# Performance work log

Hardware: AMD Instinct MI355X
Metric: run time of the kernel (lower is better)

## Reference

```python
import jax, jax.numpy as jnp
import numpy as np

N = 100000
E = 1600000
DIN = 256
DOUT = 64


def setup_inputs() -> dict:
    key = jax.random.key(0)
    ks = jax.random.split(key, 12)
    s = 1.0 / np.sqrt(DIN)
    so = 1.0 / np.sqrt(DOUT)
    return {
        "x": jax.random.normal(ks[0], (N, DIN), dtype=jnp.float32),
        "edge_index": jax.random.randint(ks[1], (2, E), 0, N, dtype=jnp.int32),
        "W_hp": jax.random.uniform(ks[2], (DIN, DOUT), jnp.float32, -s, s),
        "b_hp": jnp.zeros((DOUT,), jnp.float32),
        "W_lp": jax.random.uniform(ks[3], (DIN, DOUT), jnp.float32, -s, s),
        "b_lp": jnp.zeros((DOUT,), jnp.float32),
        "W_i": jax.random.uniform(ks[4], (DIN, DOUT), jnp.float32, -s, s),
        "b_i": jnp.zeros((DOUT,), jnp.float32),
        "w_h": jax.random.uniform(ks[5], (DOUT, 1), jnp.float32, -so, so),
        "b_h": jnp.zeros((1,), jnp.float32),
        "w_l": jax.random.uniform(ks[6], (DOUT, 1), jnp.float32, -so, so),
        "b_l": jnp.zeros((1,), jnp.float32),
        "w_i2": jax.random.uniform(ks[7], (DOUT, 1), jnp.float32, -so, so),
        "b_i2": jnp.zeros((1,), jnp.float32),
    }


def _gcn_norm(edge_index, n):
    # add self loops, symmetric GCN normalization
    ar = jnp.arange(n, dtype=edge_index.dtype)
    src = jnp.concatenate([edge_index[0], ar])
    dst = jnp.concatenate([edge_index[1], ar])
    deg = jax.ops.segment_sum(jnp.ones_like(dst, dtype=jnp.float32), dst, num_segments=n)
    dinv = jnp.where(deg > 0, jax.lax.rsqrt(jnp.maximum(deg, 1e-12)), 0.0)
    norm = dinv[src] * dinv[dst]  # [E+N]
    return src, dst, norm


def reference(x, edge_index, W_hp, b_hp, W_lp, b_lp, W_i, b_i,
              w_h, b_h, w_l, b_l, w_i2, b_i2):
    n = x.shape[0]
    src, dst, norm = _gcn_norm(edge_index, n)

    def prop(h):  # Ahat @ h via gather-scale-scatter
        return jax.ops.segment_sum(h[src] * norm[:, None], dst, num_segments=n)

    # three ACM-GCN filter branches
    xw_hp = x @ W_hp + b_hp
    H_hp = jax.nn.relu(xw_hp - prop(xw_hp))      # high-pass: (I - Ahat) X W
    H_lp = jax.nn.relu(prop(x @ W_lp + b_lp))    # low-pass:  Ahat X W
    H_i = jax.nn.relu(x @ W_i + b_i)             # identity:  X W

    # per-node sigmoid gates (mix=False path)
    a_h = jax.nn.sigmoid(H_hp @ w_h + b_h)[:, 0]
    a_l = jax.nn.sigmoid(H_lp @ w_l + b_l)[:, 0]
    a_i = jax.nn.sigmoid(H_i @ w_i2 + b_i2)[:, 0]

    # diag(alpha) @ H == broadcasted row scaling (same math, no NxN diag)
    out = a_h[:, None] * H_hp + a_l[:, None] * H_lp + a_i[:, None] * H_i
    return jax.nn.log_softmax(out, axis=1)
```

## Files before the change

kernel.cpp:

```cpp
#include <hip/hip_runtime.h>
#include <hip/hip_bf16.h>
#include <hip/hip_fp16.h>
#include <math.h>

#define DIN 256
#define DOUT 64

#define BKT_CAP 1408
#define C1_CAP 36864
#define CH1 2048
#define CH2 4096
#define NB2_PER 9

typedef __attribute__((ext_vector_type(8))) short bfrag8;
typedef __attribute__((ext_vector_type(4))) float ffrag4;
typedef __fp16 fp16x2 __attribute__((ext_vector_type(2)));

#define AS1 __attribute__((address_space(1)))
#define AS3 __attribute__((address_space(3)))

__device__ inline unsigned short f2bf(float f) {
    union { float f; unsigned u; } v; v.f = f;
    unsigned r = v.u + 0x7FFF + ((v.u >> 16) & 1);
    return (unsigned short)(r >> 16);
}
__device__ inline unsigned cvt2(float a, float b) {
    unsigned r;
    asm("v_cvt_pk_bf16_f32 %0, %1, %2" : "=v"(r) : "v"(a), "v"(b));
    return r;
}

__device__ inline float wave_sum(float v) {
    #pragma unroll
    for (int off = 32; off > 0; off >>= 1) v += __shfl_xor(v, off, 64);
    return v;
}
__device__ inline float wave_max(float v) {
    #pragma unroll
    for (int off = 32; off > 0; off >>= 1) v = fmaxf(v, __shfl_xor(v, off, 64));
    return v;
}

__device__ inline void gload16(const void* g, void* l) {
    __builtin_amdgcn_global_load_lds((const AS1 void*)g, (AS3 void*)l, 16, 0, 0);
}

union HU { unsigned u; __half2 h; };

__device__ inline void prew_body(int id, const float* __restrict__ Whp,
                                 const float* __restrict__ Wlp,
                                 const float* __restrict__ Wi,
                                 unsigned* __restrict__ wt) {
    if (id >= 8 * 192 * 4) return;
    int p = id & 3;
    int col = (id >> 2) % 192;
    int kci = id / (192 * 4);
    int s = p ^ ((col >> 1) & 3);
    int m = col >> 6, c = col & 63;
    const float* W = (m == 0) ? Whp : ((m == 1) ? Wlp : Wi);
    int k0 = kci * 32 + s * 4;
    unsigned o0 = (unsigned)f2bf(W[(k0 + 0) * 64 + c]) | ((unsigned)f2bf(W[(k0 + 1) * 64 + c]) << 16);
    unsigned o1 = (unsigned)f2bf(W[(k0 + 2) * 64 + c]) | ((unsigned)f2bf(W[(k0 + 3) * 64 + c]) << 16);
    unsigned o2 = (unsigned)f2bf(W[(k0 + 16) * 64 + c]) | ((unsigned)f2bf(W[(k0 + 17) * 64 + c]) << 16);
    unsigned o3 = (unsigned)f2bf(W[(k0 + 18) * 64 + c]) | ((unsigned)f2bf(W[(k0 + 19) * 64 + c]) << 16);
    uint4 v; v.x = o0; v.y = o1; v.z = o2; v.w = o3;
    *(uint4*)&wt[(size_t)id * 4] = v;
}

__global__ __launch_bounds__(256) void k_bin1(
    const int* __restrict__ src, const int* __restrict__ dst, int E,
    int* __restrict__ gcnt1, unsigned* __restrict__ cwords,
    const float* __restrict__ Whp, const float* __restrict__ Wlp,
    const float* __restrict__ Wi, unsigned* __restrict__ wt) {
    __shared__ int hist[4][64];
    __shared__ int roff[4][64];
    __shared__ int loff[64], gb[64];
    __shared__ unsigned words[CH1];
    __shared__ unsigned char aux[CH1];
    int t = threadIdx.x;
    int rep = t & 3;
    int base = blockIdx.x * CH1;
    int nloc = E - base;
    if (nloc > CH1) nloc = CH1;
    if (nloc < 0) nloc = 0;
    if (t < 64) { hist[0][t] = 0; hist[1][t] = 0; hist[2][t] = 0; hist[3][t] = 0; }
    __syncthreads();
    unsigned myw[8];
    short myr[8];
    signed char myb[8];
    #pragma unroll
    for (int i = 0; i < 8; ++i) {
        int idx = i * 256 + t;
        myb[i] = -1;
        if (idx < nloc) {
            int s = src[base + idx], d = dst[base + idx];
            int b = d >> 11;
            myw[i] = (unsigned)s | ((unsigned)(d & 2047) << 17);
            myb[i] = (signed char)b;
            myr[i] = (short)atomicAdd(&hist[rep][b], 1);
        }
    }
    __syncthreads();
    if (t < 64) {
        int run = 0;
        #pragma unroll
        for (int r = 0; r < 4; ++r) { roff[r][t] = run; run += hist[r][t]; }
        int v = run;
        int x = v;
        #pragma unroll
        for (int off = 1; off < 64; off <<= 1) {
            int y = __shfl_up(x, off, 64);
            if (t >= off) x += y;
        }
        loff[t] = x - v;
        gb[t] = v ? atomicAdd(&gcnt1[t], v) : 0;
    }
    __syncthreads();
    #pragma unroll
    for (int i = 0; i < 8; ++i) {
        if (myb[i] >= 0) {
            int b = myb[i];
            int pos = loff[b] + roff[rep][b] + myr[i];
            words[pos] = myw[i];
            aux[pos] = (unsigned char)b;
        }
    }
    __syncthreads();
    for (int j = t; j < nloc; j += 256) {
        int b = aux[j];
        int g = gb[b] + (j - loff[b]);
        if (g < C1_CAP) cwords[(size_t)b * C1_CAP + g] = words[j];
    }
    if (blockIdx.x < 24) prew_body(blockIdx.x * 256 + t, Whp, Wlp, Wi, wt);
}

__global__ __launch_bounds__(256) void k_bin2(
    const int* __restrict__ gcnt1, const unsigned* __restrict__ cwords,
    int* __restrict__ gcnt2, unsigned* __restrict__ bwords,
    int* __restrict__ cnt, int N) {
    __shared__ int hist[32], loff[32], gb[32];
    __shared__ int hist2k[2048];
    __shared__ unsigned words[CH2];
    __shared__ unsigned char aux[CH2];
    int t = threadIdx.x;
    int b = blockIdx.x / NB2_PER, j = blockIdx.x % NB2_PER;
    int tot = gcnt1[b];
    if (tot > C1_CAP) tot = C1_CAP;
    int base = j * CH2;
    int nloc = tot - base;
    if (nloc <= 0) return;
    if (nloc > CH2) nloc = CH2;
    if (t < 32) hist[t] = 0;
    for (int i = t; i < 2048; i += 256) hist2k[i] = 0;
    __syncthreads();
    unsigned myw[16];
    short myr[16];
    signed char myf[16];
    const unsigned* cw = cwords + (size_t)b * C1_CAP + base;
    #pragma unroll
    for (int i = 0; i < 16; ++i) {
        int idx = i * 256 + t;
        myf[i] = -1;
        if (idx < nloc) {
            unsigned w = cw[idx];
            int ld = (int)(w >> 17);
            int f = ld >> 6;
            myw[i] = (w & 0x1FFFF) | ((unsigned)(ld & 63) << 17);
            myf[i] = (signed char)f;
            myr[i] = (short)atomicAdd(&hist[f], 1);
            atomicAdd(&hist2k[ld], 1);
        }
    }
    __syncthreads();
    if (t < 32) {
        int v = hist[t];
        int x = v;
        #pragma unroll
        for (int off = 1; off < 32; off <<= 1) {
            int y = __shfl_up(x, off, 64);
            if (t >= off) x += y;
        }
        loff[t] = x - v;
        gb[t] = v ? atomicAdd(&gcnt2[b * 32 + t], v) : 0;
    }
    __syncthreads();
    #pragma unroll
    for (int i = 0; i < 16; ++i) {
        if (myf[i] >= 0) {
            int pos = loff[myf[i]] + myr[i];
            words[pos] = myw[i];
            aux[pos] = (unsigned char)myf[i];
        }
    }
    __syncthreads();
    for (int j2 = t; j2 < nloc; j2 += 256) {
        int f = aux[j2];
        int g = gb[f] + (j2 - loff[f]);
        if (g < BKT_CAP) bwords[(size_t)(b * 32 + f) * BKT_CAP + g] = words[j2];
    }
    int nbase = b * 2048;
    for (int i = t; i < 2048; i += 256) {
        int c = hist2k[i];
        if (c && nbase + i < N) atomicAdd(&cnt[nbase + i], c);
    }
}

__global__ __launch_bounds__(256) void k_gemm(
    const float* __restrict__ x, int N,
    const unsigned* __restrict__ wt,
    const float* __restrict__ bhp, const float* __restrict__ blp,
    const float* __restrict__ bi, const int* __restrict__ cnt,
    unsigned* __restrict__ xws, __half* __restrict__ xwi) {
    __shared__ __attribute__((aligned(16))) float Al[128 * 32];
    __shared__ __attribute__((aligned(16))) unsigned short Bl[192 * 32];
    int t = threadIdx.x;
    int wave = t >> 6, lane = t & 63;
    int l15 = lane & 15, lhi = lane >> 4;
    int row0 = blockIdx.x * 128;

    ffrag4 acc[2][12];
    #pragma unroll
    for (int mf = 0; mf < 2; ++mf)
        #pragma unroll
        for (int nf = 0; nf < 12; ++nf)
            acc[mf][nf] = (ffrag4){0.f, 0.f, 0.f, 0.f};

    int arow[4], achk[4];
    #pragma unroll
    for (int i = 0; i < 4; ++i) {
        int off = i * 4096 + t * 16;
        int r = off >> 7;
        int cp = (off >> 4) & 7;
        arow[i] = row0 + r < N ? row0 + r : N - 1;
        achk[i] = cp ^ (r & 7);
    }

    for (int kci = 0; kci < 8; ++kci) {
        #pragma unroll
        for (int i = 0; i < 4; ++i)
            gload16(x + (size_t)arow[i] * DIN + kci * 32 + achk[i] * 4,
                    (char*)Al + i * 4096 + wave * 1024);
        #pragma unroll
        for (int i = 0; i < 3; ++i)
            gload16(wt + (size_t)kci * 3072 + ((i * 4096 + t * 16) >> 2),
                    (char*)Bl + i * 4096 + wave * 1024);
        __syncthreads();

        union { bfrag8 v; unsigned u[4]; } af[2];
        #pragma unroll
        for (int mf = 0; mf < 2; ++mf) {
            int row = wave * 32 + mf * 16 + l15;
            int p1 = lhi ^ (row & 7);
            float4 lo = ((const float4*)Al)[row * 8 + p1];
            float4 hi = ((const float4*)Al)[row * 8 + (p1 ^ 4)];
            af[mf].u[0] = cvt2(lo.x, lo.y);
            af[mf].u[1] = cvt2(lo.z, lo.w);
            af[mf].u[2] = cvt2(hi.x, hi.y);
            af[mf].u[3] = cvt2(hi.z, hi.w);
        }
        bfrag8 bfr[12];
        #pragma unroll
        for (int nf = 0; nf < 12; ++nf) {
            int col = nf * 16 + l15;
            int p = lhi ^ ((col >> 1) & 3);
            bfr[nf] = *((const bfrag8*)Bl + col * 4 + p);
        }
        #pragma unroll
        for (int mf = 0; mf < 2; ++mf)
            #pragma unroll
            for (int nf = 0; nf < 12; ++nf)
                acc[mf][nf] = __builtin_amdgcn_mfma_f32_16x16x32_bf16(
                    af[mf].v, bfr[nf], acc[mf][nf], 0, 0, 0);
        __syncthreads();
    }

    #pragma unroll
    for (int mf = 0; mf < 2; ++mf) {
        #pragma unroll
        for (int nf = 0; nf < 4; ++nf) {
            int col = nf * 16 + l15;
            float bh_ = bhp[col], bl_ = blp[col], bi_ = bi[col];
            #pragma unroll
            for (int r = 0; r < 4; ++r) {
                int grow = row0 + wave * 32 + mf * 16 + lhi * 4 + r;
                if (grow >= N) continue;
                float dv = rsqrtf((float)cnt[grow] + 1.f);
                float hp = (acc[mf][nf][r] + bh_) * dv;
                float lp = (acc[mf][nf + 4][r] + bl_) * dv;
                union { fp16x2 p; unsigned u; } pu;
                pu.p = __builtin_amdgcn_cvt_pkrtz(hp, lp);
                xws[(size_t)grow * 64 + col] = pu.u;
                xwi[(size_t)grow * 64 + col] = __float2half(acc[mf][nf + 8][r] + bi_);
            }
        }
    }
}

__global__ __launch_bounds__(256) void k_bagg(
    const int* __restrict__ gcnt2, const unsigned* __restrict__ bwords,
    const unsigned* __restrict__ xws, const __half* __restrict__ xwi,
    const float* __restrict__ wh, const float* __restrict__ bh,
    const float* __restrict__ wl, const float* __restrict__ bl,
    const float* __restrict__ wi2, const float* __restrict__ bi2,
    float* __restrict__ out, int N) {
    __shared__ unsigned sorted[1024];
    __shared__ int h2[32], lo2[32];
    int t = threadIdx.x, bb = blockIdx.x;
    int b = bb >> 1, half = bb & 1;
    int n0 = b * 64 + half * 32;
    if (n0 >= N) return;
    int cntE = gcnt2[b];
    if (cntE > BKT_CAP) cntE = BKT_CAP;
    if (t < 32) h2[t] = 0;
    __syncthreads();
    unsigned mw[6];
    short ml[6], mr[6];
    #pragma unroll
    for (int i = 0; i < 6; ++i) {
        int idx = i * 256 + t;
        ml[i] = -1;
        if (idx < cntE) {
            unsigned w = bwords[(size_t)b * BKT_CAP + idx];
            int ld = (int)(w >> 17);
            if ((ld >> 5) == half) {
                int l5 = ld & 31;
                mw[i] = (w & 0x1FFFF) << 8;
                ml[i] = (short)l5;
                mr[i] = (short)atomicAdd(&h2[l5], 1);
            }
        }
    }
    __syncthreads();
    if (t < 32) {
        int v = h2[t];
        int x = v;
        #pragma unroll
        for (int off = 1; off < 32; off <<= 1) {
            int y = __shfl_up(x, off, 64);
            if (t >= off) x += y;
        }
        lo2[t] = x - v;
    }
    __syncthreads();
    #pragma unroll
    for (int i = 0; i < 6; ++i)
        if (ml[i] >= 0) {
            int pos = lo2[ml[i]] + mr[i];
            if (pos < 1024) sorted[pos] = mw[i];
        }
    __syncthreads();

    int wave = t >> 6, lane = t & 63;
    int h = lane >> 5, f2 = lane & 31;
    const unsigned laneoff = (unsigned)(f2 * 8);
    const char* bp = (const char*)xws;
    float wh0 = wh[f2 * 2], wh1 = wh[f2 * 2 + 1];
    float wl0 = wl[f2 * 2], wl1 = wl[f2 * 2 + 1];
    float wi0 = wi2[f2 * 2], wi1 = wi2[f2 * 2 + 1];
    float bhv = bh[0], blv = bl[0], biv = bi2[0];
    for (int ni = 0; ni < 8; ++ni) {
        int ln = wave * 8 + ni;
        int node = n0 + ln;
        if (node >= N) break;
        int c = h2[ln], e0 = lo2[ln], e1 = e0 + c;
        if (e1 > 1024) e1 = 1024;
        unsigned long long us = *(const unsigned long long*)(bp + ((unsigned)node << 8) + laneoff);
        HU z; z.u = 0;
        __half2 a0a = z.h, a0b = z.h, a1a = z.h, a1b = z.h;
        int e = e0;
        for (; e + 16 <= e1; e += 16) {
            unsigned long long v[8];
            #pragma unroll
            for (int k = 0; k < 8; ++k)
                v[k] = *(const unsigned long long*)(bp + (sorted[e + 2 * k + h] + laneoff));
            #pragma unroll
            for (int k = 0; k < 8; k += 2) {
                HU a, bq, c2, d2;
                a.u = (unsigned)v[k];      bq.u = (unsigned)(v[k] >> 32);
                c2.u = (unsigned)v[k + 1]; d2.u = (unsigned)(v[k + 1] >> 32);
                a0a = __hadd2(a0a, a.h);  a1a = __hadd2(a1a, bq.h);
                a0b = __hadd2(a0b, c2.h); a1b = __hadd2(a1b, d2.h);
            }
        }
        if (e + 8 <= e1) {
            unsigned long long v[4];
            #pragma unroll
            for (int k = 0; k < 4; ++k)
                v[k] = *(const unsigned long long*)(bp + (sorted[e + 2 * k + h] + laneoff));
            #pragma unroll
            for (int k = 0; k < 4; k += 2) {
                HU a, bq, c2, d2;
                a.u = (unsigned)v[k];      bq.u = (unsigned)(v[k] >> 32);
                c2.u = (unsigned)v[k + 1]; d2.u = (unsigned)(v[k + 1] >> 32);
                a0a = __hadd2(a0a, a.h);  a1a = __hadd2(a1a, bq.h);
                a0b = __hadd2(a0b, c2.h); a1b = __hadd2(a1b, d2.h);
            }
            e += 8;
        }
        if (e + 4 <= e1) {
            unsigned long long v[2];
            #pragma unroll
            for (int k = 0; k < 2; ++k)
                v[k] = *(const unsigned long long*)(bp + (sorted[e + 2 * k + h] + laneoff));
            HU a, bq, c2, d2;
            a.u = (unsigned)v[0];  bq.u = (unsigned)(v[0] >> 32);
            c2.u = (unsigned)v[1]; d2.u = (unsigned)(v[1] >> 32);
            a0a = __hadd2(a0a, a.h);  a1a = __hadd2(a1a, bq.h);
            a0b = __hadd2(a0b, c2.h); a1b = __hadd2(a1b, d2.h);
            e += 4;
        }
        for (; e < e1; e += 2) {
            int ei = e + h;
            if (ei < e1) {
                unsigned long long v = *(const unsigned long long*)(bp + (sorted[ei] + laneoff));
                HU a, bq;
                a.u = (unsigned)v;
                bq.u = (unsigned)(v >> 32);
                a0a = __hadd2(a0a, a.h);
                a1a = __hadd2(a1a, bq.h);
            }
        }
        __half2 acc0 = __hadd2(a0a, a0b);
        __half2 acc1 = __hadd2(a1a, a1b);
        HU c0, c1;
        c0.h = acc0; c0.u = __shfl_xor(c0.u, 32, 64);
        c1.h = acc1; c1.u = __shfl_xor(c1.u, 32, 64);
        acc0 = __hadd2(acc0, c0.h);
        acc1 = __hadd2(acc1, c1.h);
        float s_h0 = __low2float(acc0), s_l0 = __high2float(acc0);
        float s_h1 = __low2float(acc1), s_l1 = __high2float(acc1);
        float fc = (float)c + 1.f;
        float dv = rsqrtf(fc), sq = sqrtf(fc);
        HU q0, q1;
        q0.u = (unsigned)us; q1.u = (unsigned)(us >> 32);
        float xh0 = __low2float(q0.h), xl0 = __high2float(q0.h);
        float xh1 = __low2float(q1.h), xl1 = __high2float(q1.h);
        float Hh0 = fmaxf(xh0 * sq - dv * (s_h0 + xh0), 0.f);
        float Hh1 = fmaxf(xh1 * sq - dv * (s_h1 + xh1), 0.f);
        float Hl0 = fmaxf(dv * (s_l0 + xl0), 0.f);
        float Hl1 = fmaxf(dv * (s_l1 + xl1), 0.f);
        HU qi;
        qi.u = *(const unsigned*)((const char*)xwi + ((size_t)node * 128) + f2 * 4);
        float Hi0 = fmaxf(__low2float(qi.h), 0.f);
        float Hi1 = fmaxf(__high2float(qi.h), 0.f);
        float zh = 0.5f * wave_sum(Hh0 * wh0 + Hh1 * wh1) + bhv;
        float zl = 0.5f * wave_sum(Hl0 * wl0 + Hl1 * wl1) + blv;
        float zi = 0.5f * wave_sum(Hi0 * wi0 + Hi1 * wi1) + biv;
        float ah = 1.f / (1.f + expf(-zh));
        float al = 1.f / (1.f + expf(-zl));
        float ai = 1.f / (1.f + expf(-zi));
        float o0 = ah * Hh0 + al * Hl0 + ai * Hi0;
        float o1 = ah * Hh1 + al * Hl1 + ai * Hi1;
        float mx = wave_max(fmaxf(o0, o1));
        float ss = 0.5f * wave_sum(expf(o0 - mx) + expf(o1 - mx));
        float lse = mx + logf(ss);
        if (h == 0) {
            float2 r; r.x = o0 - lse; r.y = o1 - lse;
            *(float2*)&out[(size_t)node * 64 + f2 * 2] = r;
        }
    }
}

extern "C" void kernel_launch(void* const* d_in, const int* in_sizes, int n_in,
                              void* d_out, int out_size, void* d_ws, size_t ws_size,
                              hipStream_t stream) {
    const float* x   = (const float*)d_in[0];
    const int*   ei  = (const int*)d_in[1];
    const float* Whp = (const float*)d_in[2];
    const float* bhp = (const float*)d_in[3];
    const float* Wlp = (const float*)d_in[4];
    const float* blp = (const float*)d_in[5];
    const float* Wi  = (const float*)d_in[6];
    const float* bi  = (const float*)d_in[7];
    const float* wh  = (const float*)d_in[8];
    const float* bh  = (const float*)d_in[9];
    const float* wl  = (const float*)d_in[10];
    const float* bl  = (const float*)d_in[11];
    const float* wi2 = (const float*)d_in[12];
    const float* bi2 = (const float*)d_in[13];
    float* out = (float*)d_out;

    int N = in_sizes[0] / DIN;
    int E = in_sizes[1] / 2;
    const int* src = ei;
    const int* dst = ei + E;
    int nc = (N + 2047) >> 11;
    int nbuck2 = nc * 32;

    char* w = (char*)d_ws;
    size_t off = 0;
    auto alloc = [&](size_t bytes) {
        void* p = w + off;
        off += (bytes + 255) & ~size_t(255);
        return p;
    };
    int*      cnt    = (int*)alloc((size_t)N * 4);
    int*      gcnt1  = (int*)alloc(64 * 4);
    int*      gcnt2  = (int*)alloc((size_t)nbuck2 * 4);
    size_t    zero_end = off;
    unsigned* cwords = (unsigned*)alloc((size_t)nc * C1_CAP * 4);
    unsigned* bwords = (unsigned*)alloc((size_t)nbuck2 * BKT_CAP * 4);
    unsigned* xws    = (unsigned*)alloc((size_t)N * 64 * 4);
    __half*   xwi    = (__half*)alloc((size_t)N * 64 * 2);
    unsigned* wt     = (unsigned*)alloc((size_t)8 * 192 * 4 * 16);
    (void)ws_size; (void)n_in; (void)out_size;

    hipError_t e0 = hipMemsetAsync(cnt, 0, zero_end, stream); (void)e0;
    k_bin1<<<(E + CH1 - 1) / CH1, 256, 0, stream>>>(src, dst, E, gcnt1, cwords,
                                                    Whp, Wlp, Wi, wt);
    k_bin2<<<nc * NB2_PER, 256, 0, stream>>>(gcnt1, cwords, gcnt2, bwords, cnt, N);
    k_gemm<<<(N + 127) / 128, 256, 0, stream>>>(x, N, wt, bhp, blp, bi, cnt,
                                                xws, xwi);
    k_bagg<<<nbuck2 * 2, 256, 0, stream>>>(gcnt2, bwords, xws, xwi,
                                           wh, bh, wl, bl, wi2, bi2, out, N);
}
```

Measured before the change: 150.7 us.

## Replace two-pass edge binning with single-pass 1024-bucket sort and per-edge source norm

Collapses the two-level radix binning (64 coarse then 32 fine buckets) into one pass that bins edges directly into 128-node buckets, counting in-degree with global atomics per edge. The GEMM no longer scales by the destination norm; instead a new kernel builds packed fp16 source dinv values, and aggregation multiplies each gathered row by its source dinv via hfma2, with the destination scale applied at the end. Aggregation blocks grow to 512 threads handling 128 nodes. The weight preprocessing moves to its own launch. This removes a full read/write of the intermediate edge buffer, at the cost of 1.6M global atomics on cnt, two extra kernel launches, a larger LDS scan and an extra LDS array per edge in aggregation.

```diff
diff --git a/kernel.cpp b/kernel.cpp
--- a/kernel.cpp
+++ b/kernel.cpp
@@ -6,11 +6,9 @@
 #define DIN 256
 #define DOUT 64
 
-#define BKT_CAP 1408
-#define C1_CAP 36864
-#define CH1 2048
-#define CH2 4096
-#define NB2_PER 9
+#define CH1 4096
+#define NBK 1024
+#define MCAP 2560
 
 typedef __attribute__((ext_vector_type(8))) short bfrag8;
 typedef __attribute__((ext_vector_type(4))) float ffrag4;
@@ -47,10 +45,9 @@
 
 union HU { unsigned u; __half2 h; };
 
-__device__ inline void prew_body(int id, const float* __restrict__ Whp,
-                                 const float* __restrict__ Wlp,
-                                 const float* __restrict__ Wi,
-                                 unsigned* __restrict__ wt) {
+__global__ void k_prew(const float* __restrict__ Whp, const float* __restrict__ Wlp,
+                       const float* __restrict__ Wi, unsigned* __restrict__ wt) {
+    int id = blockIdx.x * 256 + threadIdx.x;
     if (id >= 8 * 192 * 4) return;
     int p = id & 3;
     int col = (id >> 2) % 192;
@@ -67,141 +64,77 @@
     *(uint4*)&wt[(size_t)id * 4] = v;
 }
 
-__global__ __launch_bounds__(256) void k_bin1(
+__global__ __launch_bounds__(512) void k_bin1(
     const int* __restrict__ src, const int* __restrict__ dst, int E,
-    int* __restrict__ gcnt1, unsigned* __restrict__ cwords,
-    const float* __restrict__ Whp, const float* __restrict__ Wlp,
-    const float* __restrict__ Wi, unsigned* __restrict__ wt) {
-    __shared__ int hist[4][64];
-    __shared__ int roff[4][64];
-    __shared__ int loff[64], gb[64];
+    int* __restrict__ cnt, int* __restrict__ gcnt, unsigned* __restrict__ mwords) {
+    __shared__ int hist[NBK], loff[NBK], gb[NBK];
+    __shared__ int sc[512];
     __shared__ unsigned words[CH1];
-    __shared__ unsigned char aux[CH1];
+    __shared__ unsigned short aux[CH1];
     int t = threadIdx.x;
-    int rep = t & 3;
     int base = blockIdx.x * CH1;
     int nloc = E - base;
     if (nloc > CH1) nloc = CH1;
     if (nloc < 0) nloc = 0;
-    if (t < 64) { hist[0][t] = 0; hist[1][t] = 0; hist[2][t] = 0; hist[3][t] = 0; }
+    for (int i = t; i < NBK; i += 512) hist[i] = 0;
     __syncthreads();
     unsigned myw[8];
-    short myr[8];
-    signed char myb[8];
+    short myr[8], myb[8];
     #pragma unroll
     for (int i = 0; i < 8; ++i) {
-        int idx = i * 256 + t;
+        int idx = i * 512 + t;
         myb[i] = -1;
         if (idx < nloc) {
             int s = src[base + idx], d = dst[base + idx];
-            int b = d >> 11;
-            myw[i] = (unsigned)s | ((unsigned)(d & 2047) << 17);
-            myb[i] = (signed char)b;
-            myr[i] = (short)atomicAdd(&hist[rep][b], 1);
-        }
-    }
-    __syncthreads();
-    if (t < 64) {
-        int run = 0;
-        #pragma unroll
-        for (int r = 0; r < 4; ++r) { roff[r][t] = run; run += hist[r][t]; }
-        int v = run;
-        int x = v;
-        #pragma unroll
-        for (int off = 1; off < 64; off <<= 1) {
-            int y = __shfl_up(x, off, 64);
-            if (t >= off) x += y;
-        }
-        loff[t] = x - v;
-        gb[t] = v ? atomicAdd(&gcnt1[t], v) : 0;
+            int b = d >> 7;
+            myw[i] = (unsigned)s | ((unsigned)(d & 127) << 17);
+            myb[i] = (short)b;
+            myr[i] = (short)atomicAdd(&hist[b], 1);
+            atomicAdd(&cnt[d], 1);
+        }
+    }
+    __syncthreads();
+    int part = hist[t * 2] + hist[t * 2 + 1];
+    sc[t] = part; __syncthreads();
+    for (int off = 1; off < 512; off <<= 1) {
+        int x = (t >= off) ? sc[t - off] : 0;
+        __syncthreads();
+        sc[t] += x;
+        __syncthreads();
+    }
+    int run = sc[t] - part;
+    loff[t * 2] = run;
+    run += hist[t * 2];
+    loff[t * 2 + 1] = run;
+    __syncthreads();
+    for (int i = t; i < NBK; i += 512) {
+        int c = hist[i];
+        gb[i] = c ? atomicAdd(&gcnt[i], c) : 0;
     }
     __syncthreads();
     #pragma unroll
     for (int i = 0; i < 8; ++i) {
         if (myb[i] >= 0) {
-            int b = myb[i];
-            int pos = loff[b] + roff[rep][b] + myr[i];
+            int pos = loff[myb[i]] + myr[i];
             words[pos] = myw[i];
-            aux[pos] = (unsigned char)b;
-        }
-    }
-    __syncthreads();
-    for (int j = t; j < nloc; j += 256) {
+            aux[pos] = (unsigned short)myb[i];
+        }
+    }
+    __syncthreads();
+    for (int j = t; j < nloc; j += 512) {
         int b = aux[j];
         int g = gb[b] + (j - loff[b]);
-        if (g < C1_CAP) cwords[(size_t)b * C1_CAP + g] = words[j];
-    }
-    if (blockIdx.x < 24) prew_body(blockIdx.x * 256 + t, Whp, Wlp, Wi, wt);
-}
-
-__global__ __launch_bounds__(256) void k_bin2(
-    const int* __restrict__ gcnt1, const unsigned* __restrict__ cwords,
-    int* __restrict__ gcnt2, unsigned* __restrict__ bwords,
-    int* __restrict__ cnt, int N) {
-    __shared__ int hist[32], loff[32], gb[32];
-    __shared__ int hist2k[2048];
-    __shared__ unsigned words[CH2];
-    __shared__ unsigned char aux[CH2];
-    int t = threadIdx.x;
-    int b = blockIdx.x / NB2_PER, j = blockIdx.x % NB2_PER;
-    int tot = gcnt1[b];
-    if (tot > C1_CAP) tot = C1_CAP;
-    int base = j * CH2;
-    int nloc = tot - base;
-    if (nloc <= 0) return;
-    if (nloc > CH2) nloc = CH2;
-    if (t < 32) hist[t] = 0;
-    for (int i = t; i < 2048; i += 256) hist2k[i] = 0;
-    __syncthreads();
-    unsigned myw[16];
-    short myr[16];
-    signed char myf[16];
-    const unsigned* cw = cwords + (size_t)b * C1_CAP + base;
-    #pragma unroll
-    for (int i = 0; i < 16; ++i) {
-        int idx = i * 256 + t;
-        myf[i] = -1;
-        if (idx < nloc) {
-            unsigned w = cw[idx];
-            int ld = (int)(w >> 17);
-            int f = ld >> 6;
-            myw[i] = (w & 0x1FFFF) | ((unsigned)(ld & 63) << 17);
-            myf[i] = (signed char)f;
-            myr[i] = (short)atomicAdd(&hist[f], 1);
-            atomicAdd(&hist2k[ld], 1);
-        }
-    }
-    __syncthreads();
-    if (t < 32) {
-        int v = hist[t];
-        int x = v;
-        #pragma unroll
-        for (int off = 1; off < 32; off <<= 1) {
-            int y = __shfl_up(x, off, 64);
-            if (t >= off) x += y;
-        }
-        loff[t] = x - v;
-        gb[t] = v ? atomicAdd(&gcnt2[b * 32 + t], v) : 0;
-    }
-    __syncthreads();
-    #pragma unroll
-    for (int i = 0; i < 16; ++i) {
-        if (myf[i] >= 0) {
-            int pos = loff[myf[i]] + myr[i];
-            words[pos] = myw[i];
-            aux[pos] = (unsigned char)myf[i];
-        }
-    }
-    __syncthreads();
-    for (int j2 = t; j2 < nloc; j2 += 256) {
-        int f = aux[j2];
-        int g = gb[f] + (j2 - loff[f]);
-        if (g < BKT_CAP) bwords[(size_t)(b * 32 + f) * BKT_CAP + g] = words[j2];
-    }
-    int nbase = b * 2048;
-    for (int i = t; i < 2048; i += 256) {
-        int c = hist2k[i];
-        if (c && nbase + i < N) atomicAdd(&cnt[nbase + i], c);
+        if (g < MCAP) mwords[(size_t)b * MCAP + g] = words[j];
+    }
+}
+
+__global__ void k_dinv2(const int* __restrict__ cnt, unsigned* __restrict__ dinv2, int N) {
+    int i = blockIdx.x * blockDim.x + threadIdx.x;
+    if (i < N) {
+        float dv = rsqrtf((float)cnt[i] + 1.f);
+        union { fp16x2 p; unsigned u; } pu;
+        pu.p = __builtin_amdgcn_cvt_pkrtz(dv, dv);
+        dinv2[i] = pu.u;
     }
 }
 
@@ -209,7 +142,7 @@
     const float* __restrict__ x, int N,
     const unsigned* __restrict__ wt,
     const float* __restrict__ bhp, const float* __restrict__ blp,
-    const float* __restrict__ bi, const int* __restrict__ cnt,
+    const float* __restrict__ bi,
     unsigned* __restrict__ xws, __half* __restrict__ xwi) {
     __shared__ __attribute__((aligned(16))) float Al[128 * 32];
     __shared__ __attribute__((aligned(16))) unsigned short Bl[192 * 32];
@@ -284,9 +217,8 @@
             for (int r = 0; r < 4; ++r) {
                 int grow = row0 + wave * 32 + mf * 16 + lhi * 4 + r;
                 if (grow >= N) continue;
-                float dv = rsqrtf((float)cnt[grow] + 1.f);
-                float hp = (acc[mf][nf][r] + bh_) * dv;
-                float lp = (acc[mf][nf + 4][r] + bl_) * dv;
+                float hp = acc[mf][nf][r] + bh_;
+                float lp = acc[mf][nf + 4][r] + bl_;
                 union { fp16x2 p; unsigned u; } pu;
                 pu.p = __builtin_amdgcn_cvt_pkrtz(hp, lp);
                 xws[(size_t)grow * 64 + col] = pu.u;
@@ -296,57 +228,57 @@
     }
 }
 
-__global__ __launch_bounds__(256) void k_bagg(
-    const int* __restrict__ gcnt2, const unsigned* __restrict__ bwords,
+__global__ __launch_bounds__(512) void k_bagg(
+    const int* __restrict__ gcnt, const unsigned* __restrict__ mwords,
     const unsigned* __restrict__ xws, const __half* __restrict__ xwi,
+    const unsigned* __restrict__ dinv2,
     const float* __restrict__ wh, const float* __restrict__ bh,
     const float* __restrict__ wl, const float* __restrict__ bl,
     const float* __restrict__ wi2, const float* __restrict__ bi2,
     float* __restrict__ out, int N) {
-    __shared__ unsigned sorted[1024];
-    __shared__ int h2[32], lo2[32];
-    int t = threadIdx.x, bb = blockIdx.x;
-    int b = bb >> 1, half = bb & 1;
-    int n0 = b * 64 + half * 32;
+    __shared__ unsigned sorted[MCAP];
+    __shared__ unsigned sdv[MCAP];
+    __shared__ int h2[128], lo2[128], sc2[128];
+    int t = threadIdx.x, b = blockIdx.x;
+    int n0 = b << 7;
     if (n0 >= N) return;
-    int cntE = gcnt2[b];
-    if (cntE > BKT_CAP) cntE = BKT_CAP;
-    if (t < 32) h2[t] = 0;
-    __syncthreads();
-    unsigned mw[6];
-    short ml[6], mr[6];
-    #pragma unroll
-    for (int i = 0; i < 6; ++i) {
-        int idx = i * 256 + t;
+    int cntE = gcnt[b];
+    if (cntE > MCAP) cntE = MCAP;
+    if (t < 128) h2[t] = 0;
+    __syncthreads();
+    unsigned mw[5];
+    short ml[5], mr[5];
+    #pragma unroll
+    for (int i = 0; i < 5; ++i) {
+        int idx = i * 512 + t;
         ml[i] = -1;
         if (idx < cntE) {
-            unsigned w = bwords[(size_t)b * BKT_CAP + idx];
+            unsigned w = mwords[(size_t)b * MCAP + idx];
             int ld = (int)(w >> 17);
-            if ((ld >> 5) == half) {
-                int l5 = ld & 31;
-                mw[i] = (w & 0x1FFFF) << 8;
-                ml[i] = (short)l5;
-                mr[i] = (short)atomicAdd(&h2[l5], 1);
-            }
-        }
-    }
-    __syncthreads();
-    if (t < 32) {
-        int v = h2[t];
-        int x = v;
-        #pragma unroll
-        for (int off = 1; off < 32; off <<= 1) {
-            int y = __shfl_up(x, off, 64);
-            if (t >= off) x += y;
-        }
-        lo2[t] = x - v;
-    }
-    __syncthreads();
-    #pragma unroll
-    for (int i = 0; i < 6; ++i)
+            mw[i] = (w & 0x1FFFF) << 8;
+            ml[i] = (short)ld;
+            mr[i] = (short)atomicAdd(&h2[ld], 1);
+        }
+    }
+    __syncthreads();
+    if (t < 128) sc2[t] = h2[t];
+    __syncthreads();
+    for (int off = 1; off < 128; off <<= 1) {
+        int x = (t < 128 && t >= off) ? sc2[t - off] : 0;
+        __syncthreads();
+        if (t < 128) sc2[t] += x;
+        __syncthreads();
+    }
+    if (t < 128) lo2[t] = sc2[t] - h2[t];
+    __syncthreads();
+    #pragma unroll
+    for (int i = 0; i < 5; ++i)
         if (ml[i] >= 0) {
             int pos = lo2[ml[i]] + mr[i];
-            if (pos < 1024) sorted[pos] = mw[i];
+            if (pos < MCAP) {
+                sorted[pos] = mw[i];
+                sdv[pos] = dinv2[mw[i] >> 8];
+            }
         }
     __syncthreads();
 
@@ -358,66 +290,82 @@
     float wl0 = wl[f2 * 2], wl1 = wl[f2 * 2 + 1];
     float wi0 = wi2[f2 * 2], wi1 = wi2[f2 * 2 + 1];
     float bhv = bh[0], blv = bl[0], biv = bi2[0];
-    for (int ni = 0; ni < 8; ++ni) {
-        int ln = wave * 8 + ni;
+    for (int ni = 0; ni < 16; ++ni) {
+        int ln = wave * 16 + ni;
         int node = n0 + ln;
         if (node >= N) break;
         int c = h2[ln], e0 = lo2[ln], e1 = e0 + c;
-        if (e1 > 1024) e1 = 1024;
+        if (e1 > MCAP) e1 = MCAP;
         unsigned long long us = *(const unsigned long long*)(bp + ((unsigned)node << 8) + laneoff);
         HU z; z.u = 0;
         __half2 a0a = z.h, a0b = z.h, a1a = z.h, a1b = z.h;
         int e = e0;
         for (; e + 16 <= e1; e += 16) {
             unsigned long long v[8];
-            #pragma unroll
-            for (int k = 0; k < 8; ++k)
-                v[k] = *(const unsigned long long*)(bp + (sorted[e + 2 * k + h] + laneoff));
+            unsigned dd[8];
+            #pragma unroll
+            for (int k = 0; k < 8; ++k) {
+                int idx = e + 2 * k + h;
+                dd[k] = sdv[idx];
+                v[k] = *(const unsigned long long*)(bp + (sorted[idx] + laneoff));
+            }
             #pragma unroll
             for (int k = 0; k < 8; k += 2) {
-                HU a, bq, c2, d2;
+                HU a, bq, c2, d2, w0, w1;
                 a.u = (unsigned)v[k];      bq.u = (unsigned)(v[k] >> 32);
                 c2.u = (unsigned)v[k + 1]; d2.u = (unsigned)(v[k + 1] >> 32);
-                a0a = __hadd2(a0a, a.h);  a1a = __hadd2(a1a, bq.h);
-                a0b = __hadd2(a0b, c2.h); a1b = __hadd2(a1b, d2.h);
+                w0.u = dd[k]; w1.u = dd[k + 1];
+                a0a = __hfma2(a.h, w0.h, a0a);  a1a = __hfma2(bq.h, w0.h, a1a);
+                a0b = __hfma2(c2.h, w1.h, a0b); a1b = __hfma2(d2.h, w1.h, a1b);
             }
         }
         if (e + 8 <= e1) {
             unsigned long long v[4];
-            #pragma unroll
-            for (int k = 0; k < 4; ++k)
-                v[k] = *(const unsigned long long*)(bp + (sorted[e + 2 * k + h] + laneoff));
+            unsigned dd[4];
+            #pragma unroll
+            for (int k = 0; k < 4; ++k) {
+                int idx = e + 2 * k + h;
+                dd[k] = sdv[idx];
+                v[k] = *(const unsigned long long*)(bp + (sorted[idx] + laneoff));
+            }
             #pragma unroll
             for (int k = 0; k < 4; k += 2) {
-                HU a, bq, c2, d2;
+                HU a, bq, c2, d2, w0, w1;
                 a.u = (unsigned)v[k];      bq.u = (unsigned)(v[k] >> 32);
                 c2.u = (unsigned)v[k + 1]; d2.u = (unsigned)(v[k + 1] >> 32);
-                a0a = __hadd2(a0a, a.h);  a1a = __hadd2(a1a, bq.h);
-                a0b = __hadd2(a0b, c2.h); a1b = __hadd2(a1b, d2.h);
+                w0.u = dd[k]; w1.u = dd[k + 1];
+                a0a = __hfma2(a.h, w0.h, a0a);  a1a = __hfma2(bq.h, w0.h, a1a);
+                a0b = __hfma2(c2.h, w1.h, a0b); a1b = __hfma2(d2.h, w1.h, a1b);
             }
             e += 8;
         }
         if (e + 4 <= e1) {
             unsigned long long v[2];
-            #pragma unroll
-            for (int k = 0; k < 2; ++k)
-                v[k] = *(const unsigned long long*)(bp + (sorted[e + 2 * k + h] + laneoff));
-            HU a, bq, c2, d2;
+            unsigned dd[2];
+            #pragma unroll
+            for (int k = 0; k < 2; ++k) {
+                int idx = e + 2 * k + h;
+                dd[k] = sdv[idx];
+                v[k] = *(const unsigned long long*)(bp + (sorted[idx] + laneoff));
+            }
+            HU a, bq, c2, d2, w0, w1;
             a.u = (unsigned)v[0];  bq.u = (unsigned)(v[0] >> 32);
             c2.u = (unsigned)v[1]; d2.u = (unsigned)(v[1] >> 32);
-            a0a = __hadd2(a0a, a.h);  a1a = __hadd2(a1a, bq.h);
-            a0b = __hadd2(a0b, c2.h); a1b = __hadd2(a1b, d2.h);
+            w0.u = dd[0]; w1.u = dd[1];
+            a0a = __hfma2(a.h, w0.h, a0a);  a1a = __hfma2(bq.h, w0.h, a1a);
+            a0b = __hfma2(c2.h, w1.h, a0b); a1b = __hfma2(d2.h, w1.h, a1b);
             e += 4;
         }
         for (; e < e1; e += 2) {
             int ei = e + h;
             if (ei < e1) {
                 unsigned long long v = *(const unsigned long long*)(bp + (sorted[ei] + laneoff));
-                HU a, bq;
+                HU a, bq, w0;
                 a.u = (unsigned)v;
                 bq.u = (unsigned)(v >> 32);
-                a0a = __hadd2(a0a, a.h);
-                a1a = __hadd2(a1a, bq.h);
+                w0.u = sdv[ei];
+                a0a = __hfma2(a.h, w0.h, a0a);
+                a1a = __hfma2(bq.h, w0.h, a1a);
             }
         }
         __half2 acc0 = __hadd2(a0a, a0b);
@@ -429,16 +377,15 @@
         acc1 = __hadd2(acc1, c1.h);
         float s_h0 = __low2float(acc0), s_l0 = __high2float(acc0);
         float s_h1 = __low2float(acc1), s_l1 = __high2float(acc1);
-        float fc = (float)c + 1.f;
-        float dv = rsqrtf(fc), sq = sqrtf(fc);
+        float dv = rsqrtf((float)c + 1.f);
         HU q0, q1;
         q0.u = (unsigned)us; q1.u = (unsigned)(us >> 32);
         float xh0 = __low2float(q0.h), xl0 = __high2float(q0.h);
         float xh1 = __low2float(q1.h), xl1 = __high2float(q1.h);
-        float Hh0 = fmaxf(xh0 * sq - dv * (s_h0 + xh0), 0.f);
-        float Hh1 = fmaxf(xh1 * sq - dv * (s_h1 + xh1), 0.f);
-        float Hl0 = fmaxf(dv * (s_l0 + xl0), 0.f);
-        float Hl1 = fmaxf(dv * (s_l1 + xl1), 0.f);
+        float Hh0 = fmaxf(xh0 - dv * (s_h0 + dv * xh0), 0.f);
+        float Hh1 = fmaxf(xh1 - dv * (s_h1 + dv * xh1), 0.f);
+        float Hl0 = fmaxf(dv * (s_l0 + dv * xl0), 0.f);
+        float Hl1 = fmaxf(dv * (s_l1 + dv * xl1), 0.f);
         HU qi;
         qi.u = *(const unsigned*)((const char*)xwi + ((size_t)node * 128) + f2 * 4);
         float Hi0 = fmaxf(__low2float(qi.h), 0.f);
@@ -484,8 +431,7 @@
     int E = in_sizes[1] / 2;
     const int* src = ei;
     const int* dst = ei + E;
-    int nc = (N + 2047) >> 11;
-    int nbuck2 = nc * 32;
+    int nbuck = (N + 127) >> 7;
 
     char* w = (char*)d_ws;
     size_t off = 0;
@@ -495,22 +441,20 @@
         return p;
     };
     int*      cnt    = (int*)alloc((size_t)N * 4);
-    int*      gcnt1  = (int*)alloc(64 * 4);
-    int*      gcnt2  = (int*)alloc((size_t)nbuck2 * 4);
+    int*      gcnt   = (int*)alloc((size_t)NBK * 4);
     size_t    zero_end = off;
-    unsigned* cwords = (unsigned*)alloc((size_t)nc * C1_CAP * 4);
-    unsigned* bwords = (unsigned*)alloc((size_t)nbuck2 * BKT_CAP * 4);
+    unsigned* mwords = (unsigned*)alloc((size_t)nbuck * MCAP * 4);
     unsigned* xws    = (unsigned*)alloc((size_t)N * 64 * 4);
     __half*   xwi    = (__half*)alloc((size_t)N * 64 * 2);
     unsigned* wt     = (unsigned*)alloc((size_t)8 * 192 * 4 * 16);
+    unsigned* dinv2  = (unsigned*)alloc((size_t)N * 4);
     (void)ws_size; (void)n_in; (void)out_size;
 
     hipError_t e0 = hipMemsetAsync(cnt, 0, zero_end, stream); (void)e0;
-    k_bin1<<<(E + CH1 - 1) / CH1, 256, 0, stream>>>(src, dst, E, gcnt1, cwords,
-                                                    Whp, Wlp, Wi, wt);
-    k_bin2<<<nc * NB2_PER, 256, 0, stream>>>(gcnt1, cwords, gcnt2, bwords, cnt, N);
-    k_gemm<<<(N + 127) / 128, 256, 0, stream>>>(x, N, wt, bhp, blp, bi, cnt,
-                                                xws, xwi);
-    k_bagg<<<nbuck2 * 2, 256, 0, stream>>>(gcnt2, bwords, xws, xwi,
-                                           wh, bh, wl, bl, wi2, bi2, out, N);
-}
+    k_prew<<<24, 256, 0, stream>>>(Whp, Wlp, Wi, wt);
+    k_bin1<<<(E + CH1 - 1) / CH1, 512, 0, stream>>>(src, dst, E, cnt, gcnt, mwords);
+    k_dinv2<<<(N + 255) / 256, 256, 0, stream>>>(cnt, dinv2, N);
+    k_gemm<<<(N + 127) / 128, 256, 0, stream>>>(x, N, wt, bhp, blp, bi, xws, xwi);
+    k_bagg<<<nbuck, 512, 0, stream>>>(gcnt, mwords, xws, xwi, dinv2,
+                                      wh, bh, wl, bl, wi2, bi2, out, N);
+}
```

Result: slower. 205.2 us (+36.1%).
